# Kernel tuning notes

Measured on AMD Instinct MI355X. Metric: run time of the kernel, lower is better.

## Reference

```python
import jax, jax.numpy as jnp
import numpy as np

B, S, DIM = 2, 2048, 4096
HQ, HKV, HD = 32, 8, 128
N_REP = HQ // HKV
MAX_S = 2048
ROPE_BASE = 10000.0


def rotate_half(x):
    half = x.shape[-1] // 2
    return jnp.concatenate([-x[..., half:], x[..., :half]], axis=-1)


def setup_inputs() -> dict:
    key = jax.random.key(0)
    ks = jax.random.split(key, 8)
    x = jax.random.normal(ks[0], (B, S, DIM), dtype=jnp.float32)
    Wq = jax.random.normal(ks[1], (HQ * HD, DIM), dtype=jnp.float32) * 0.02
    bq = jax.random.normal(ks[2], (HQ * HD,), dtype=jnp.float32) * 0.02
    Wk = jax.random.normal(ks[3], (HKV * HD, DIM), dtype=jnp.float32) * 0.02
    bk = jax.random.normal(ks[4], (HKV * HD,), dtype=jnp.float32) * 0.02
    Wv = jax.random.normal(ks[5], (HKV * HD, DIM), dtype=jnp.float32) * 0.02
    bv = jax.random.normal(ks[6], (HKV * HD,), dtype=jnp.float32) * 0.02
    Wo = jax.random.normal(ks[7], (DIM, HQ * HD), dtype=jnp.float32) * 0.02
    # RoPE tables (HF convention: angles duplicated across both halves)
    inv_freq = 1.0 / (ROPE_BASE ** (jnp.arange(0, HD, 2, dtype=jnp.float32) / HD))
    pos = jnp.arange(S, dtype=jnp.float32)
    ang = pos[:, None] * inv_freq[None, :]              # [S, HD/2]
    emb = jnp.concatenate([ang, ang], axis=-1)          # [S, HD]
    cos, sin = jnp.cos(emb), jnp.sin(emb)
    # static KV cache, zero-initialized as in the module
    cache_k = jnp.zeros((B, HKV, MAX_S, HD), dtype=jnp.float32)
    cache_v = jnp.zeros((B, HKV, MAX_S, HD), dtype=jnp.float32)
    # causal additive mask
    causal = jnp.tril(jnp.ones((S, S), dtype=bool))
    mask = jnp.where(causal, 0.0, -1e9).astype(jnp.float32)[None, None]  # [1,1,S,S]
    return {"x": x, "cos": cos, "sin": sin, "Wq": Wq, "bq": bq, "Wk": Wk,
            "bk": bk, "Wv": Wv, "bv": bv, "Wo": Wo, "cache_k": cache_k,
            "cache_v": cache_v, "mask": mask, "start_pos": 0}


def reference(x, cos, sin, Wq, bq, Wk, bk, Wv, bv, Wo, cache_k, cache_v, mask, start_pos):
    bsz, seqlen, _ = x.shape
    scaling = 1.0 / jnp.sqrt(jnp.float32(HD))
    # QKV projections
    xq = (jnp.einsum('bsd,ed->bse', x, Wq) + bq).reshape(bsz, seqlen, HQ, HD).transpose(0, 2, 1, 3)
    xk = (jnp.einsum('bsd,ed->bse', x, Wk) + bk).reshape(bsz, seqlen, HKV, HD).transpose(0, 2, 1, 3)
    xv = (jnp.einsum('bsd,ed->bse', x, Wv) + bv).reshape(bsz, seqlen, HKV, HD).transpose(0, 2, 1, 3)
    # RoPE
    c = cos[None, None]  # [1,1,S,HD]
    s = sin[None, None]
    xq = xq * c + rotate_half(xq) * s
    xk = xk * c + rotate_half(xk) * s
    # static KV-cache append + slice (start_pos is a Python int)
    cache_k = jax.lax.dynamic_update_slice(cache_k, xk, (0, 0, start_pos, 0))
    cache_v = jax.lax.dynamic_update_slice(cache_v, xv, (0, 0, start_pos, 0))
    keys = cache_k[:, :, :start_pos + seqlen]     # [B,HKV,K,HD]
    values = cache_v[:, :, :start_pos + seqlen]
    # GQA: repeat kv heads (repeat_interleave over head dim)
    keys = jnp.repeat(keys, N_REP, axis=1)        # [B,HQ,K,HD]
    values = jnp.repeat(values, N_REP, axis=1)
    # SDPA with additive mask
    scores = jnp.einsum('bhqd,bhkd->bhqk', xq, keys) * scaling + mask
    attn = jax.nn.softmax(scores, axis=-1)
    out = jnp.einsum('bhqk,bhkd->bhqd', attn, values)
    out = out.transpose(0, 2, 1, 3).reshape(bsz, seqlen, HQ * HD)
    return jnp.einsum('bse,de->bsd', out, Wo)
```

## Files before the change

kernel.cpp:

```cpp
#include <hip/hip_runtime.h>

typedef _Float16 half8 __attribute__((ext_vector_type(8)));
typedef _Float16 half4 __attribute__((ext_vector_type(4)));
typedef float floatx4 __attribute__((ext_vector_type(4)));
typedef float floatx16 __attribute__((ext_vector_type(16)));

#define SWZ(r) ((((r) & 7) << 1) | (((r) >> 3) & 1))

__device__ __forceinline__ void gld16(const void* g, void* l) {
  __builtin_amdgcn_global_load_lds(
      (const __attribute__((address_space(1))) unsigned int*)g,
      (__attribute__((address_space(3))) unsigned int*)l, 16, 0, 0);
}

__global__ void convert_all(const float* __restrict__ x, const float* __restrict__ Wq,
                            const float* __restrict__ Wk, const float* __restrict__ Wv,
                            const float* __restrict__ Wo, const float* __restrict__ bq,
                            const float* __restrict__ bk, const float* __restrict__ bv,
                            _Float16* __restrict__ xb, _Float16* __restrict__ wqkv,
                            _Float16* __restrict__ wo_b, float* __restrict__ biasc) {
  long i = (long)blockIdx.x * 256 + threadIdx.x;
  const long N0 = 2097152, N1 = N0 + 2097152, N2 = N1 + 524288, N3 = N2 + 524288,
             N4 = N3 + 2097152;
  const float* s;
  _Float16* d;
  long j;
  if (i < N0) { s = x; d = xb; j = i; }
  else if (i < N1) { s = Wq; d = wqkv; j = i - N0; }
  else if (i < N2) { s = Wk; d = wqkv + (size_t)4096 * 4096; j = i - N1; }
  else if (i < N3) { s = Wv; d = wqkv + (size_t)5120 * 4096; j = i - N2; }
  else if (i < N4) { s = Wo; d = wo_b; j = i - N3; }
  else {
    long k = i - N4;
    if (k < 4096) biasc[k] = bq[k];
    else if (k < 5120) biasc[k] = bk[k - 4096];
    else if (k < 6144) biasc[k] = bv[k - 5120];
    return;
  }
  float4 a = ((const float4*)s)[2 * j];
  float4 b2 = ((const float4*)s)[2 * j + 1];
  half8 h;
  h[0] = (_Float16)a.x; h[1] = (_Float16)a.y; h[2] = (_Float16)a.z; h[3] = (_Float16)a.w;
  h[4] = (_Float16)b2.x; h[5] = (_Float16)b2.y; h[6] = (_Float16)b2.z; h[7] = (_Float16)b2.w;
  ((half8*)d)[j] = h;
}

template <typename OutT, bool HasBias>
__global__ __launch_bounds__(512, 2) void gemm256(const _Float16* __restrict__ A,
                                                  const _Float16* __restrict__ B,
                                                  const float* __restrict__ bias,
                                                  OutT* __restrict__ C, int M, int N, int K) {
  __shared__ _Float16 as[2][256 * 64];
  __shared__ _Float16 bs[2][256 * 64];
  const int tid = threadIdx.x;
  const int w = tid >> 6, lane = tid & 63;
  const int quad = lane >> 4, l16 = lane & 15;
  const int sw7 = l16 & 7;
  const int M0 = blockIdx.y * 256, N0 = blockIdx.x * 256;
  const int wm = (w >> 2) * 128, wn = (w & 3) * 64;
  const int NT = K >> 6;

  floatx4 acc[8][4];
#pragma unroll
  for (int i = 0; i < 8; ++i)
#pragma unroll
    for (int j = 0; j < 4; ++j) acc[i][j] = (floatx4){0.f, 0.f, 0.f, 0.f};

  const int sr = tid >> 3;
  const int csw = ((tid & 7) ^ (sr & 7)) * 8;
  const _Float16* Ag[4];
  const _Float16* Bg[4];
#pragma unroll
  for (int j = 0; j < 4; ++j) {
    Ag[j] = A + (size_t)(M0 + j * 64 + sr) * K + csw;
    Bg[j] = B + (size_t)(N0 + j * 64 + sr) * K + csw;
  }

#define STA(p, t, j) gld16(Ag[j] + (size_t)(t) * 64, &as[p][(j) * 4096 + w * 512])
#define STB(p, t, j) gld16(Bg[j] + (size_t)(t) * 64, &bs[p][(j) * 4096 + w * 512])

#define FRA(p, q, mi, kd) \
  (*(const half8*)&as[p][(wm + (q) * 32 + (mi) * 16 + l16) * 64 + ((((kd) * 4 + quad) ^ sw7) * 8)])
#define FRB(p, ni, kd) \
  (*(const half8*)&bs[p][(wn + (ni) * 16 + l16) * 64 + ((((kd) * 4 + quad) ^ sw7) * 8)])

#define LD_A(p, q)                                   \
  _Pragma("unroll") for (int kd = 0; kd < 2; ++kd)   \
  _Pragma("unroll") for (int mi = 0; mi < 2; ++mi)   \
      af[mi][kd] = FRA(p, q, mi, kd);

#define LD_B(p)                                      \
  _Pragma("unroll") for (int kd = 0; kd < 2; ++kd)   \
  _Pragma("unroll") for (int ni = 0; ni < 4; ++ni)   \
      bf[ni][kd] = FRB(p, ni, kd);

#define PH_COMPUTE(q)                                                                  \
  __builtin_amdgcn_s_barrier();                                                        \
  asm volatile("s_waitcnt lgkmcnt(0)" ::: "memory");                                   \
  __builtin_amdgcn_sched_barrier(0);                                                   \
  __builtin_amdgcn_s_setprio(1);                                                       \
  _Pragma("unroll") for (int kd = 0; kd < 2; ++kd)                                     \
  _Pragma("unroll") for (int mi = 0; mi < 2; ++mi)                                     \
  _Pragma("unroll") for (int ni = 0; ni < 4; ++ni)                                     \
      acc[(q) * 2 + mi][ni] = __builtin_amdgcn_mfma_f32_16x16x32_f16(                  \
          af[mi][kd], bf[ni][kd], acc[(q) * 2 + mi][ni], 0, 0, 0);                     \
  __builtin_amdgcn_s_setprio(0);

  half8 bf[4][2], af[2][2];

  STA(0, 0, 0); STA(0, 0, 1); STA(0, 0, 2); STA(0, 0, 3);
  STB(0, 0, 0); STB(0, 0, 1); STB(0, 0, 2); STB(0, 0, 3);
  STB(1, 1, 0); STB(1, 1, 1); STB(1, 1, 2); STB(1, 1, 3);
  asm volatile("s_waitcnt vmcnt(4)" ::: "memory");
  __builtin_amdgcn_s_barrier();

  for (int t = 0; t < NT; t += 2) {
    const int t2 = (t + 2 < NT) ? t + 2 : t;
    const int t3 = (t + 3 < NT) ? t + 3 : t + 1;

    LD_B(0); LD_A(0, 0);
    STA(1, t + 1, 0); STA(1, t + 1, 1); STA(1, t + 1, 2); STA(1, t + 1, 3);
    PH_COMPUTE(0);
    __builtin_amdgcn_s_barrier();

    LD_A(0, 1);
    STB(0, t2, 0); STB(0, t2, 1);
    PH_COMPUTE(1);
    __builtin_amdgcn_s_barrier();

    LD_A(0, 2);
    STB(0, t2, 2); STB(0, t2, 3);
    PH_COMPUTE(2);
    __builtin_amdgcn_s_barrier();

    LD_A(0, 3);
    PH_COMPUTE(3);
    asm volatile("s_waitcnt vmcnt(4)" ::: "memory");
    __builtin_amdgcn_sched_barrier(0);
    __builtin_amdgcn_s_barrier();

    LD_B(1); LD_A(1, 0);
    STA(0, t2, 0); STA(0, t2, 1);
    PH_COMPUTE(0);
    __builtin_amdgcn_s_barrier();

    LD_A(1, 1);
    STA(0, t2, 2); STA(0, t2, 3);
    PH_COMPUTE(1);
    __builtin_amdgcn_s_barrier();

    LD_A(1, 2);
    STB(1, t3, 0); STB(1, t3, 1);
    PH_COMPUTE(2);
    __builtin_amdgcn_s_barrier();

    LD_A(1, 3);
    STB(1, t3, 2); STB(1, t3, 3);
    PH_COMPUTE(3);
    asm volatile("s_waitcnt vmcnt(4)" ::: "memory");
    __builtin_amdgcn_sched_barrier(0);
    __builtin_amdgcn_s_barrier();
  }

#pragma unroll
  for (int mf = 0; mf < 8; ++mf)
#pragma unroll
    for (int ni = 0; ni < 4; ++ni) {
      int row = M0 + wm + mf * 16 + quad * 4;
      int col = N0 + wn + ni * 16 + l16;
      float bvv = HasBias ? bias[col] : 0.f;
#pragma unroll
      for (int r = 0; r < 4; ++r) C[(size_t)(row + r) * N + col] = (OutT)(acc[mf][ni][r] + bvv);
    }
#undef STA
#undef STB
#undef FRA
#undef FRB
#undef LD_A
#undef LD_B
#undef PH_COMPUTE
}

__global__ void rope_qk(const _Float16* __restrict__ qkv, const float* __restrict__ cosb,
                        const float* __restrict__ sinb, _Float16* __restrict__ q_r,
                        _Float16* __restrict__ k_r) {
  int t = blockIdx.x * 256 + threadIdx.x;
  int d = t & 63;
  int r = t >> 6;
  int hh = r % 40;
  int r2 = r / 40;
  int s = r2 & 2047;
  int b = r2 >> 11;
  size_t mrow = (size_t)(b * 2048 + s) * 6144;
  float c = cosb[s * 128 + d], sn = sinb[s * 128 + d];
  if (hh < 32) {
    size_t base = mrow + hh * 128 + d;
    float x1 = (float)qkv[base], x2 = (float)qkv[base + 64];
    const float sc = 0.12751744737079736f;
    float o1 = (x1 * c - x2 * sn) * sc;
    float o2 = (x2 * c + x1 * sn) * sc;
    size_t ob = ((size_t)((b * 32 + hh) * 2048 + s)) * 128 + d;
    q_r[ob] = (_Float16)o1;
    q_r[ob + 64] = (_Float16)o2;
  } else {
    int hk = hh - 32;
    size_t base = mrow + 4096 + hk * 128 + d;
    float x1 = (float)qkv[base], x2 = (float)qkv[base + 64];
    float o1 = x1 * c - x2 * sn;
    float o2 = x2 * c + x1 * sn;
    size_t ob = ((size_t)((b * 8 + hk) * 2048 + s)) * 128 + d;
    k_r[ob] = (_Float16)o1;
    k_r[ob + 64] = (_Float16)o2;
  }
}

__global__ void v_transpose(const _Float16* __restrict__ qkv, _Float16* __restrict__ v_t) {
  __shared__ _Float16 tile[32][33];
  int st = blockIdx.x * 32, dt = blockIdx.y * 32, bh = blockIdx.z;
  int tx = threadIdx.x & 31, ty = threadIdx.x >> 5;
  int b = bh >> 3, hv = bh & 7;
#pragma unroll
  for (int j = 0; j < 4; ++j) {
    int s = st + ty + j * 8;
    tile[ty + j * 8][tx] = qkv[(size_t)(b * 2048 + s) * 6144 + 5120 + hv * 128 + dt + tx];
  }
  __syncthreads();
#pragma unroll
  for (int j = 0; j < 4; ++j)
    v_t[((size_t)bh * 128 + dt + ty + j * 8) * 2048 + st + tx] = tile[tx][ty + j * 8];
}

__global__ __launch_bounds__(256, 2) void attn_kernel(const _Float16* __restrict__ q_r,
                                                      const _Float16* __restrict__ k_r,
                                                      const _Float16* __restrict__ v_t,
                                                      _Float16* __restrict__ att) {
  __shared__ __align__(16) _Float16 kt[128 * 128];
  __shared__ __align__(16) _Float16 vt[128 * 128];
  const int tid = threadIdx.x;
  const int w = tid >> 6, lane = tid & 63;
  const int l32 = lane & 31, hi = lane >> 5;
  const int qb = 15 - blockIdx.x;
  const int h = blockIdx.y, b = blockIdx.z;
  const int q0 = qb * 128;
  const _Float16* qh = q_r + ((size_t)(b * 32 + h) * 2048) * 128;
  const _Float16* kh = k_r + ((size_t)(b * 8 + (h >> 2)) * 2048) * 128;
  const _Float16* vh = v_t + ((size_t)(b * 8 + (h >> 2)) * 128) * 2048;

  const int ql = w * 32 + l32;
  const int myq = q0 + ql;
  const int swq = SWZ(ql);
  const int swl = SWZ(l32);

  half8 bq[8];
#pragma unroll
  for (int kd = 0; kd < 8; ++kd)
    bq[kd] = *(const half8*)&qh[(size_t)myq * 128 + kd * 16 + hi * 8];

  floatx16 oacc[4];
#pragma unroll
  for (int di = 0; di < 4; ++di)
#pragma unroll
    for (int j = 0; j < 16; ++j) oacc[di][j] = 0.f;
  float mrun = -1e30f, lrun = 0.f;

  const int srow0 = tid >> 4, sgrp = tid & 15;

  for (int kti = 0; kti <= qb; ++kti) {
    __syncthreads();
    const _Float16* kg = kh + (size_t)kti * 128 * 128;
#pragma unroll
    for (int c = 0; c < 8; ++c) {
      int row = srow0 + c * 16;
      int gc = (sgrp ^ SWZ(row)) * 8;
      gld16(kg + row * 128 + gc, &kt[w * 512 + c * 2048]);
    }
#pragma unroll
    for (int c = 0; c < 8; ++c) {
      int row = srow0 + c * 16;
      int gc = (sgrp ^ SWZ(row)) * 8;
      gld16(vh + (size_t)row * 2048 + kti * 128 + gc, &vt[w * 512 + c * 2048]);
    }
    __syncthreads();

    floatx16 sacc[4];
#pragma unroll
    for (int ni = 0; ni < 4; ++ni)
#pragma unroll
      for (int j = 0; j < 16; ++j) sacc[ni][j] = 0.f;
#pragma unroll
    for (int ni = 0; ni < 4; ++ni) {
      int rb = (ni * 32 + l32) * 128;
#pragma unroll
      for (int kd = 0; kd < 8; ++kd) {
        half8 ka = *(const half8*)&kt[rb + (((kd * 2 + hi) ^ swl) * 8)];
        sacc[ni] = __builtin_amdgcn_mfma_f32_32x32x16_f16(ka, bq[kd], sacc[ni], 0, 0, 0);
      }
    }

    if (kti == qb) {
#pragma unroll
      for (int ni = 0; ni < 4; ++ni)
#pragma unroll
        for (int g = 0; g < 4; ++g) {
          int kvb = kti * 128 + ni * 32 + g * 8 + hi * 4;
#pragma unroll
          for (int t = 0; t < 4; ++t)
            if (kvb + t > myq) sacc[ni][g * 4 + t] = -1e30f;
        }
    }

    float tm = -1e30f;
#pragma unroll
    for (int ni = 0; ni < 4; ++ni)
#pragma unroll
      for (int j = 0; j < 16; ++j) tm = fmaxf(tm, sacc[ni][j]);
    tm = fmaxf(tm, __shfl_xor(tm, 32));
    float nm = fmaxf(mrun, tm);
    float al = exp2f(mrun - nm);
    mrun = nm;
    float ts = 0.f;
#pragma unroll
    for (int ni = 0; ni < 4; ++ni)
#pragma unroll
      for (int j = 0; j < 16; ++j) {
        float p = exp2f(sacc[ni][j] - nm);
        sacc[ni][j] = p;
        ts += p;
      }
    ts += __shfl_xor(ts, 32);
    lrun = lrun * al + ts;
#pragma unroll
    for (int di = 0; di < 4; ++di)
#pragma unroll
      for (int j = 0; j < 16; ++j) oacc[di][j] *= al;

    __syncthreads();

#pragma unroll
    for (int ni = 0; ni < 4; ++ni)
#pragma unroll
      for (int g = 0; g < 4; ++g) {
        half4 p4;
#pragma unroll
        for (int t = 0; t < 4; ++t) p4[t] = (_Float16)sacc[ni][g * 4 + t];
        *(half4*)&kt[ql * 128 + (((ni * 4 + g) ^ swq) * 8) + hi * 4] = p4;
      }

#pragma unroll
    for (int ks = 0; ks < 8; ++ks) {
      half8 pb = *(const half8*)&kt[ql * 128 + (((ks * 2 + hi) ^ swq) * 8)];
#pragma unroll
      for (int di = 0; di < 4; ++di) {
        int rv = (di * 32 + l32) * 128;
        half8 va = *(const half8*)&vt[rv + (((ks * 2 + hi) ^ swl) * 8)];
        oacc[di] = __builtin_amdgcn_mfma_f32_32x32x16_f16(va, pb, oacc[di], 0, 0, 0);
      }
    }
  }

  float inv = 1.f / lrun;
  _Float16* ob = att + ((size_t)b * 2048 + myq) * 4096 + h * 128;
#pragma unroll
  for (int di = 0; di < 4; ++di)
#pragma unroll
    for (int g = 0; g < 4; ++g) {
      half4 o4;
#pragma unroll
      for (int t = 0; t < 4; ++t) o4[t] = (_Float16)(oacc[di][g * 4 + t] * inv);
      *(half4*)&ob[di * 32 + g * 8 + hi * 4] = o4;
    }
}

extern "C" void kernel_launch(void* const* d_in, const int* in_sizes, int n_in, void* d_out,
                              int out_size, void* d_ws, size_t ws_size, hipStream_t stream) {
  const float* x = (const float*)d_in[0];
  const float* cosb = (const float*)d_in[1];
  const float* sinb = (const float*)d_in[2];
  const float* Wq = (const float*)d_in[3];
  const float* bq = (const float*)d_in[4];
  const float* Wk = (const float*)d_in[5];
  const float* bk = (const float*)d_in[6];
  const float* Wv = (const float*)d_in[7];
  const float* bv = (const float*)d_in[8];
  const float* Wo = (const float*)d_in[9];
  float* out = (float*)d_out;

  char* p = (char*)d_ws;
  _Float16* xb = (_Float16*)p;   p += (size_t)4096 * 4096 * 2;
  _Float16* wqkv = (_Float16*)p; p += (size_t)6144 * 4096 * 2;
  _Float16* wo_b = (_Float16*)p; p += (size_t)4096 * 4096 * 2;
  _Float16* qkv = (_Float16*)p;  p += (size_t)4096 * 6144 * 2;
  _Float16* q_r = (_Float16*)p;  p += (size_t)2 * 32 * 2048 * 128 * 2;
  _Float16* k_r = (_Float16*)p;  p += (size_t)2 * 8 * 2048 * 128 * 2;
  _Float16* v_t = (_Float16*)p;  p += (size_t)2 * 8 * 128 * 2048 * 2;
  _Float16* att = (_Float16*)p;  p += (size_t)4096 * 4096 * 2;
  float* biasc = (float*)p;      p += 6144 * 4;

  convert_all<<<28696, 256, 0, stream>>>(x, Wq, Wk, Wv, Wo, bq, bk, bv, xb, wqkv, wo_b, biasc);

  gemm256<_Float16, true><<<dim3(24, 16), 512, 0, stream>>>(xb, wqkv, biasc, qkv, 4096, 6144, 4096);
  rope_qk<<<40960, 256, 0, stream>>>(qkv, cosb, sinb, q_r, k_r);
  v_transpose<<<dim3(64, 4, 16), 256, 0, stream>>>(qkv, v_t);
  attn_kernel<<<dim3(16, 32, 2), 256, 0, stream>>>(q_r, k_r, v_t, att);
  gemm256<float, false><<<dim3(16, 16), 512, 0, stream>>>(att, wo_b, nullptr, out, 4096, 4096, 4096);
}
```

Baseline: 928.4 us.

## Double-buffer attention KV tiles and use simpler 128x128 GEMM for QKV

The attention kernel now streams K/V in 64-row tiles into double-buffered shared memory, prefetching the next tile while computing the current one. This hides global load latency behind the MFMA work. The QKV projection switches from the 256x256 pipelined GEMM to a new, simpler 128x128 single-buffered GEMM using 16x16x32 MFMA, and a vmcnt(0) wait is added at the end of the old GEMM. The new GEMM has no load/compute overlap, and the smaller attention tiles add more barriers per key position.

```diff
diff --git a/kernel.cpp b/kernel.cpp
--- a/kernel.cpp
+++ b/kernel.cpp
@@ -46,6 +46,87 @@
 }
 
 template <typename OutT, bool HasBias>
+__global__ __launch_bounds__(256) void gemm_bt(const _Float16* __restrict__ A,
+                                               const _Float16* __restrict__ B,
+                                               const float* __restrict__ bias,
+                                               OutT* __restrict__ C, int M, int N, int K) {
+  __shared__ _Float16 as[128 * 64];
+  __shared__ _Float16 bs[128 * 64];
+  const int tid = threadIdx.x;
+  const int w = tid >> 6, lane = tid & 63;
+  const int quad = lane >> 4, l16 = lane & 15;
+  const int M0 = blockIdx.y * 128, N0 = blockIdx.x * 128;
+  const int wm = (w >> 1) * 64, wn = (w & 1) * 64;
+
+  floatx4 acc[4][4];
+#pragma unroll
+  for (int i = 0; i < 4; ++i)
+#pragma unroll
+    for (int j = 0; j < 4; ++j) acc[i][j] = (floatx4){0.f, 0.f, 0.f, 0.f};
+
+  const int sr = tid >> 3, g0 = tid & 7;
+  const int csw = (g0 ^ (sr & 7)) * 8;
+  const _Float16* Ag[4];
+  const _Float16* Bg[4];
+  _Float16* asd[4];
+  _Float16* bsd[4];
+#pragma unroll
+  for (int c = 0; c < 4; ++c) {
+    Ag[c] = A + (size_t)(M0 + c * 32 + sr) * K + csw;
+    Bg[c] = B + (size_t)(N0 + c * 32 + sr) * K + csw;
+    asd[c] = &as[(c * 32 + w * 8) * 64];
+    bsd[c] = &bs[(c * 32 + w * 8) * 64];
+  }
+
+  int aoff[4][2], boff[4][2];
+#pragma unroll
+  for (int mi = 0; mi < 4; ++mi)
+#pragma unroll
+    for (int kd = 0; kd < 2; ++kd) {
+      int ra = wm + mi * 16 + l16;
+      aoff[mi][kd] = ra * 64 + (((kd * 4 + quad) ^ (ra & 7)) * 8);
+      int rb = wn + mi * 16 + l16;
+      boff[mi][kd] = rb * 64 + (((kd * 4 + quad) ^ (rb & 7)) * 8);
+    }
+
+  for (int kk = 0; kk < K; kk += 64) {
+    __syncthreads();
+#pragma unroll
+    for (int c = 0; c < 4; ++c) gld16(Ag[c] + kk, asd[c]);
+#pragma unroll
+    for (int c = 0; c < 4; ++c) gld16(Bg[c] + kk, bsd[c]);
+    __syncthreads();
+#pragma unroll
+    for (int kd = 0; kd < 2; ++kd) {
+      half8 af[4], bf[4];
+#pragma unroll
+      for (int i = 0; i < 4; ++i) af[i] = *(const half8*)&as[aoff[i][kd]];
+#pragma unroll
+      for (int i = 0; i < 4; ++i) bf[i] = *(const half8*)&bs[boff[i][kd]];
+#pragma unroll
+      for (int mi = 0; mi < 4; ++mi)
+#pragma unroll
+        for (int ni = 0; ni < 4; ++ni)
+          acc[mi][ni] = __builtin_amdgcn_mfma_f32_16x16x32_f16(af[mi], bf[ni], acc[mi][ni], 0, 0, 0);
+    }
+  }
+
+#pragma unroll
+  for (int mi = 0; mi < 4; ++mi)
+#pragma unroll
+    for (int ni = 0; ni < 4; ++ni) {
+      int row = M0 + wm + mi * 16 + quad * 4;
+      int col = N0 + wn + ni * 16 + l16;
+      float bvv = HasBias ? bias[col] : 0.f;
+#pragma unroll
+      for (int r = 0; r < 4; ++r) {
+        float v = acc[mi][ni][r] + bvv;
+        C[(size_t)(row + r) * N + col] = (OutT)v;
+      }
+    }
+}
+
+template <typename OutT, bool HasBias>
 __global__ __launch_bounds__(512, 2) void gemm256(const _Float16* __restrict__ A,
                                                   const _Float16* __restrict__ B,
                                                   const float* __restrict__ bias,
@@ -161,6 +242,7 @@
     __builtin_amdgcn_sched_barrier(0);
     __builtin_amdgcn_s_barrier();
   }
+  asm volatile("s_waitcnt vmcnt(0)" ::: "memory");
 
 #pragma unroll
   for (int mf = 0; mf < 8; ++mf)
@@ -234,8 +316,8 @@
                                                       const _Float16* __restrict__ k_r,
                                                       const _Float16* __restrict__ v_t,
                                                       _Float16* __restrict__ att) {
-  __shared__ __align__(16) _Float16 kt[128 * 128];
-  __shared__ __align__(16) _Float16 vt[128 * 128];
+  __shared__ __align__(16) _Float16 kbuf[2][64 * 128];
+  __shared__ __align__(16) _Float16 vbuf[2][128 * 64];
   const int tid = threadIdx.x;
   const int w = tid >> 6, lane = tid & 63;
   const int l32 = lane & 31, hi = lane >> 5;
@@ -248,7 +330,7 @@
 
   const int ql = w * 32 + l32;
   const int myq = q0 + ql;
-  const int swq = SWZ(ql);
+  const int swq7 = ql & 7;
   const int swl = SWZ(l32);
 
   half8 bq[8];
@@ -263,46 +345,56 @@
     for (int j = 0; j < 16; ++j) oacc[di][j] = 0.f;
   float mrun = -1e30f, lrun = 0.f;
 
-  const int srow0 = tid >> 4, sgrp = tid & 15;
-
-  for (int kti = 0; kti <= qb; ++kti) {
+  const int krow = tid >> 4, kgrp = tid & 15;
+  const int vrow = tid >> 3, vgrp = tid & 7;
+
+#define STAGE_KV(p, t)                                                                     \
+  do {                                                                                     \
+    const _Float16* kg_ = kh + (size_t)(t) * 64 * 128;                                     \
+    _Pragma("unroll") for (int c = 0; c < 4; ++c) {                                        \
+      int row = c * 16 + krow;                                                             \
+      gld16(kg_ + row * 128 + ((kgrp ^ SWZ(row)) * 8), &kbuf[p][(c * 16 + w * 4) * 128]);  \
+    }                                                                                      \
+    _Pragma("unroll") for (int c = 0; c < 4; ++c) {                                        \
+      int row = c * 32 + vrow;                                                             \
+      gld16(vh + (size_t)row * 2048 + (size_t)(t) * 64 + ((vgrp ^ (row & 7)) * 8),         \
+            &vbuf[p][(c * 32 + w * 8) * 64]);                                              \
+    }                                                                                      \
+  } while (0)
+
+  const int nsteps = 2 * qb + 2;
+  STAGE_KV(0, 0);
+
+  for (int s = 0; s < nsteps; ++s) {
+    const int cur = s & 1;
     __syncthreads();
-    const _Float16* kg = kh + (size_t)kti * 128 * 128;
-#pragma unroll
-    for (int c = 0; c < 8; ++c) {
-      int row = srow0 + c * 16;
-      int gc = (sgrp ^ SWZ(row)) * 8;
-      gld16(kg + row * 128 + gc, &kt[w * 512 + c * 2048]);
-    }
-#pragma unroll
-    for (int c = 0; c < 8; ++c) {
-      int row = srow0 + c * 16;
-      int gc = (sgrp ^ SWZ(row)) * 8;
-      gld16(vh + (size_t)row * 2048 + kti * 128 + gc, &vt[w * 512 + c * 2048]);
-    }
+    const int sn = (s + 1 < nsteps) ? s + 1 : s;
+    STAGE_KV(cur ^ 1, sn);
+    asm volatile("s_waitcnt vmcnt(8)" ::: "memory");
     __syncthreads();
 
-    floatx16 sacc[4];
-#pragma unroll
-    for (int ni = 0; ni < 4; ++ni)
+    floatx16 sacc[2];
+#pragma unroll
+    for (int ni = 0; ni < 2; ++ni)
 #pragma unroll
       for (int j = 0; j < 16; ++j) sacc[ni][j] = 0.f;
 #pragma unroll
-    for (int ni = 0; ni < 4; ++ni) {
+    for (int ni = 0; ni < 2; ++ni) {
       int rb = (ni * 32 + l32) * 128;
 #pragma unroll
       for (int kd = 0; kd < 8; ++kd) {
-        half8 ka = *(const half8*)&kt[rb + (((kd * 2 + hi) ^ swl) * 8)];
+        half8 ka = *(const half8*)&kbuf[cur][rb + (((kd * 2 + hi) ^ swl) * 8)];
         sacc[ni] = __builtin_amdgcn_mfma_f32_32x32x16_f16(ka, bq[kd], sacc[ni], 0, 0, 0);
       }
     }
 
-    if (kti == qb) {
-#pragma unroll
-      for (int ni = 0; ni < 4; ++ni)
+    if (s >= 2 * qb) {
+      int kv0 = s * 64;
+#pragma unroll
+      for (int ni = 0; ni < 2; ++ni)
 #pragma unroll
         for (int g = 0; g < 4; ++g) {
-          int kvb = kti * 128 + ni * 32 + g * 8 + hi * 4;
+          int kvb = kv0 + ni * 32 + g * 8 + hi * 4;
 #pragma unroll
           for (int t = 0; t < 4; ++t)
             if (kvb + t > myq) sacc[ni][g * 4 + t] = -1e30f;
@@ -311,7 +403,7 @@
 
     float tm = -1e30f;
 #pragma unroll
-    for (int ni = 0; ni < 4; ++ni)
+    for (int ni = 0; ni < 2; ++ni)
 #pragma unroll
       for (int j = 0; j < 16; ++j) tm = fmaxf(tm, sacc[ni][j]);
     tm = fmaxf(tm, __shfl_xor(tm, 32));
@@ -320,7 +412,7 @@
     mrun = nm;
     float ts = 0.f;
 #pragma unroll
-    for (int ni = 0; ni < 4; ++ni)
+    for (int ni = 0; ni < 2; ++ni)
 #pragma unroll
       for (int j = 0; j < 16; ++j) {
         float p = exp2f(sacc[ni][j] - nm);
@@ -337,26 +429,27 @@
     __syncthreads();
 
 #pragma unroll
-    for (int ni = 0; ni < 4; ++ni)
+    for (int ni = 0; ni < 2; ++ni)
 #pragma unroll
       for (int g = 0; g < 4; ++g) {
         half4 p4;
 #pragma unroll
         for (int t = 0; t < 4; ++t) p4[t] = (_Float16)sacc[ni][g * 4 + t];
-        *(half4*)&kt[ql * 128 + (((ni * 4 + g) ^ swq) * 8) + hi * 4] = p4;
+        *(half4*)&kbuf[cur][ql * 64 + (((ni * 4 + g) ^ swq7) * 8) + hi * 4] = p4;
       }
 
 #pragma unroll
-    for (int ks = 0; ks < 8; ++ks) {
-      half8 pb = *(const half8*)&kt[ql * 128 + (((ks * 2 + hi) ^ swq) * 8)];
+    for (int ks = 0; ks < 4; ++ks) {
+      half8 pb = *(const half8*)&kbuf[cur][ql * 64 + (((ks * 2 + hi) ^ swq7) * 8)];
 #pragma unroll
       for (int di = 0; di < 4; ++di) {
-        int rv = (di * 32 + l32) * 128;
-        half8 va = *(const half8*)&vt[rv + (((ks * 2 + hi) ^ swl) * 8)];
+        int rv = (di * 32 + l32) * 64;
+        half8 va = *(const half8*)&vbuf[cur][rv + (((ks * 2 + hi) ^ (l32 & 7)) * 8)];
         oacc[di] = __builtin_amdgcn_mfma_f32_32x32x16_f16(va, pb, oacc[di], 0, 0, 0);
       }
     }
   }
+  asm volatile("s_waitcnt vmcnt(0)" ::: "memory");
 
   float inv = 1.f / lrun;
   _Float16* ob = att + ((size_t)b * 2048 + myq) * 4096 + h * 128;
@@ -369,6 +462,7 @@
       for (int t = 0; t < 4; ++t) o4[t] = (_Float16)(oacc[di][g * 4 + t] * inv);
       *(half4*)&ob[di * 32 + g * 8 + hi * 4] = o4;
     }
+#undef STAGE_KV
 }
 
 extern "C" void kernel_launch(void* const* d_in, const int* in_sizes, int n_in, void* d_out,
@@ -398,7 +492,7 @@
 
   convert_all<<<28696, 256, 0, stream>>>(x, Wq, Wk, Wv, Wo, bq, bk, bv, xb, wqkv, wo_b, biasc);
 
-  gemm256<_Float16, true><<<dim3(24, 16), 512, 0, stream>>>(xb, wqkv, biasc, qkv, 4096, 6144, 4096);
+  gemm_bt<_Float16, true><<<dim3(48, 32), 256, 0, stream>>>(xb, wqkv, biasc, qkv, 4096, 6144, 4096);
   rope_qk<<<40960, 256, 0, stream>>>(qkv, cosb, sinb, q_r, k_r);
   v_transpose<<<dim3(64, 4, 16), 256, 0, stream>>>(qkv, v_t);
   attn_kernel<<<dim3(16, 32, 2), 256, 0, stream>>>(q_r, k_r, v_t, att);
```

New measurement: 881.2 us. 5.1% less time.
